# Performance work log

Measured on AMD Instinct MI355X. Metric: run time of the kernel, lower is better.

Reference implementation:

```python
import jax, jax.numpy as jnp
import numpy as np

N_NODES = 100_000
N_EDGES = 20_000   # hyperedges
NNZ = 2_000_000    # incidence pairs
F = 128
BN_EPS = 1e-5


def setup_inputs() -> dict:
    key = jax.random.key(0)
    ks = jax.random.split(key, 6)
    x_0 = jax.random.normal(ks[0], (N_NODES, F), dtype=jnp.float32)
    x_1 = jax.random.normal(ks[1], (N_EDGES, F), dtype=jnp.float32)
    node_idx = jax.random.randint(ks[2], (NNZ,), 0, N_NODES, dtype=jnp.int32)
    edge_idx = jax.random.randint(ks[3], (NNZ,), 0, N_EDGES, dtype=jnp.int32)
    W_nh = jax.random.normal(ks[4], (F, F), dtype=jnp.float32) / np.float32(np.sqrt(F))
    b_nh = jnp.zeros((F,), jnp.float32)
    W_en = jax.random.normal(ks[5], (F, 2 * F), dtype=jnp.float32) / np.float32(np.sqrt(2 * F))
    b_en = jnp.zeros((F,), jnp.float32)
    ones = jnp.ones((F,), jnp.float32)
    zeros = jnp.zeros((F,), jnp.float32)
    return {
        "x_0": x_0, "x_1": x_1, "node_idx": node_idx, "edge_idx": edge_idx,
        "W_nh": W_nh, "b_nh": b_nh, "W_en": W_en, "b_en": b_en,
        "bn0_gamma": ones, "bn0_beta": zeros, "bn0_mean": zeros, "bn0_var": ones,
        "bn1_gamma": ones, "bn1_beta": zeros, "bn1_mean": zeros, "bn1_var": ones,
    }


def _bn_eval(x, gamma, beta, mean, var):
    # BatchNorm1d in eval mode: normalize with running stats.
    return (x - mean) * (gamma * jax.lax.rsqrt(var + BN_EPS)) + beta


def reference(x_0, x_1, node_idx, edge_idx, W_nh, b_nh, W_en, b_en,
              bn0_gamma, bn0_beta, bn0_mean, bn0_var,
              bn1_gamma, bn1_beta, bn1_mean, bn1_var):
    # --- node -> hyperedge messenger ---
    # per-node message: sigmoid(Linear(x_0))  [n_nodes, F]
    node_messages = jax.nn.sigmoid(x_0 @ W_nh.T + b_nh)
    # gather over incidence list, scatter-sum onto hyperedges  [n_edges, F]
    node_msg_agg = jax.ops.segment_sum(node_messages[node_idx], edge_idx,
                                       num_segments=N_EDGES)

    # --- hyperedge -> node messenger ---
    # per-hyperedge message: sigmoid(Linear(cat(x_1, agg node msgs)))  [n_edges, F]
    he_messages = jax.nn.sigmoid(
        jnp.concatenate([x_1, node_msg_agg], axis=1) @ W_en.T + b_en)
    # gather per incidence, scatter-sum onto nodes  [n_nodes, F]
    he_msg_agg = jax.ops.segment_sum(he_messages[edge_idx], node_idx,
                                     num_segments=N_NODES)

    # --- updates (eval mode: feature dropout is identity) ---
    x0_out = jax.nn.sigmoid(
        _bn_eval(x_0, bn0_gamma, bn0_beta, bn0_mean, bn0_var) + he_msg_agg)
    x1_out = jax.nn.sigmoid(
        _bn_eval(x_1, bn1_gamma, bn1_beta, bn1_mean, bn1_var) + node_msg_agg)
    return (x0_out, x1_out)
```

## Files before the change

kernel.cpp:

```cpp
#include <hip/hip_runtime.h>
#include <hip/hip_bf16.h>
#include <math.h>

#define NNODES 100000
#define NEDGES 20000
#define NNZ_   2000000
#define FDIM   128
#define BN_EPS 1e-5f

#define NBUCK 256
#define CAP   9216
#define BPB_E 79
#define BPB_N 391
#define SH_E  17
#define SH_N  15
#define NPART 8
#define PSLICE 12500

typedef __attribute__((ext_vector_type(8))) short bf16x8_t;
typedef __attribute__((ext_vector_type(4))) float f32x4_t;
typedef __attribute__((ext_vector_type(8))) unsigned short u16x8_t;

__device__ __forceinline__ float sigmoidf_(float x) {
    return 1.0f / (1.0f + __expf(-x));
}
__device__ __forceinline__ float bf2f(unsigned short u) {
    return __uint_as_float(((unsigned)u) << 16);
}
__device__ __forceinline__ unsigned short f2bf(float f) {
    __hip_bfloat16 h = __float2bfloat16(f);
    return *reinterpret_cast<unsigned short*>(&h);
}

__global__ __launch_bounds__(256) void prep_w(
    const float* __restrict__ W_nh, const float* __restrict__ W_en,
    unsigned short* __restrict__ Wnh_bf, float* __restrict__ WTen)
{
    int idx = blockIdx.x * blockDim.x + threadIdx.x;
    if (idx < FDIM * FDIM) {
        Wnh_bf[idx] = f2bf(W_nh[idx]);
    } else {
        int j = idx - FDIM * FDIM;
        if (j >= 2 * FDIM * FDIM) return;
        int k = j >> 7, c = j & 127;
        WTen[j] = W_en[c * 2 * FDIM + k];
    }
}

__global__ __launch_bounds__(256) void gemm1_mfma(
    const float* __restrict__ x0, const unsigned short* __restrict__ Wb,
    const float* __restrict__ bias, unsigned short* __restrict__ out)
{
    __shared__ unsigned short As[32][FDIM + 8];
    const int tid  = threadIdx.x;
    const int row0 = blockIdx.x * 32;
    {
        int r = tid >> 3, c0 = (tid & 7) * 16;
        const float* src = x0 + (size_t)(row0 + r) * FDIM + c0;
        unsigned short* dst = &As[r][c0];
        #pragma unroll
        for (int i = 0; i < 4; i++) {
            float4 v = *(const float4*)(src + i * 4);
            dst[i * 4 + 0] = f2bf(v.x);
            dst[i * 4 + 1] = f2bf(v.y);
            dst[i * 4 + 2] = f2bf(v.z);
            dst[i * 4 + 3] = f2bf(v.w);
        }
    }
    __syncthreads();
    const int wave  = tid >> 6;
    const int lane  = tid & 63;
    const int mhalf = wave & 1;
    const int nhalf = wave >> 1;
    const int lm    = lane & 15;
    const int quad  = lane >> 4;
    f32x4_t acc[4] = {};
    #pragma unroll
    for (int ks = 0; ks < 4; ks++) {
        bf16x8_t a = *(const bf16x8_t*)&As[mhalf * 16 + lm][ks * 32 + quad * 8];
        #pragma unroll
        for (int nt = 0; nt < 4; nt++) {
            int n = nhalf * 64 + nt * 16 + lm;
            bf16x8_t b = *(const bf16x8_t*)(Wb + (size_t)n * FDIM + ks * 32 + quad * 8);
            acc[nt] = __builtin_amdgcn_mfma_f32_16x16x32_bf16(a, b, acc[nt], 0, 0, 0);
        }
    }
    const int mbase = row0 + mhalf * 16 + quad * 4;
    #pragma unroll
    for (int nt = 0; nt < 4; nt++) {
        int n = nhalf * 64 + nt * 16 + lm;
        float bv = bias[n];
        #pragma unroll
        for (int r2 = 0; r2 < 4; r2++) {
            out[(size_t)(mbase + r2) * FDIM + n] = f2bf(sigmoidf_(acc[nt][r2] + bv));
        }
    }
}

__global__ __launch_bounds__(256, 2) void gemm_sig_bf16(
    const float* __restrict__ A1, const float* __restrict__ A2,
    const float* __restrict__ WT, const float* __restrict__ bias,
    unsigned short* __restrict__ out)
{
    constexpr int K = 256, BK = 64;
    __shared__ float As[32][BK + 4];
    __shared__ float Ws[BK][FDIM];
    const int tid  = threadIdx.x;
    const int row0 = blockIdx.x * 32;
    const int tcol = tid & 31;
    const int trow = tid >> 5;
    float acc[4][4] = {};
    for (int kk = 0; kk < K; kk += BK) {
        const float* Asrc = (kk < FDIM) ? A1 : A2;
        const int koff    = (kk < FDIM) ? kk : kk - FDIM;
        #pragma unroll
        for (int i = 0; i < 2; i++) {
            int l = tid + i * 256;
            int r = l >> 4, j = l & 15;
            float4 v = *(const float4*)(Asrc + (size_t)(row0 + r) * FDIM + koff + j * 4);
            *(float4*)&As[r][j * 4] = v;
        }
        #pragma unroll
        for (int i = 0; i < 8; i++) {
            int l = tid + i * 256;
            int k = l >> 5, j = l & 31;
            float4 v = *(const float4*)(WT + (size_t)(kk + k) * FDIM + j * 4);
            *(float4*)&Ws[k][j * 4] = v;
        }
        __syncthreads();
        #pragma unroll
        for (int k = 0; k < BK; k += 4) {
            float4 a[4];
            #pragma unroll
            for (int r = 0; r < 4; r++)
                a[r] = *(const float4*)&As[trow * 4 + r][k];
            #pragma unroll
            for (int kq = 0; kq < 4; kq++) {
                float4 w = *(const float4*)&Ws[k + kq][tcol * 4];
                #pragma unroll
                for (int r = 0; r < 4; r++) {
                    float av = (kq == 0) ? a[r].x : (kq == 1) ? a[r].y
                             : (kq == 2) ? a[r].z : a[r].w;
                    acc[r][0] += av * w.x;
                    acc[r][1] += av * w.y;
                    acc[r][2] += av * w.z;
                    acc[r][3] += av * w.w;
                }
            }
        }
        __syncthreads();
    }
    float4 bv = *(const float4*)(bias + tcol * 4);
    #pragma unroll
    for (int r = 0; r < 4; r++) {
        int row = row0 + trow * 4 + r;
        ushort4 o;
        o.x = f2bf(sigmoidf_(acc[r][0] + bv.x));
        o.y = f2bf(sigmoidf_(acc[r][1] + bv.y));
        o.z = f2bf(sigmoidf_(acc[r][2] + bv.z));
        o.w = f2bf(sigmoidf_(acc[r][3] + bv.w));
        *(ushort4*)(out + (size_t)row * FDIM + tcol * 4) = o;
    }
}

__global__ __launch_bounds__(1024) void bucket_scatter(
    const int* __restrict__ ni, const int* __restrict__ ei,
    unsigned* __restrict__ buck_e, unsigned* __restrict__ buck_n,
    int* __restrict__ gcur_e, int* __restrict__ gcur_n)
{
    __shared__ int lh_e[NBUCK], lh_n[NBUCK], lb_e[NBUCK], lb_n[NBUCK];
    const int t = threadIdx.x;
    if (t < NBUCK) { lh_e[t] = 0; lh_n[t] = 0; }
    __syncthreads();
    unsigned ent_e[4], ent_n[4];
    int be[4], bn[4], re[4], rn[4];
    const int base = blockIdx.x * 4096;
    #pragma unroll
    for (int j = 0; j < 4; j++) {
        int i = base + j * 1024 + t;
        if (i < NNZ_) {
            unsigned n = (unsigned)ni[i], e = (unsigned)ei[i];
            ent_e[j] = (e << SH_E) | n;  be[j] = (int)(e / BPB_E);
            ent_n[j] = (n << SH_N) | e;  bn[j] = (int)(n / BPB_N);
            re[j] = atomicAdd(&lh_e[be[j]], 1);
            rn[j] = atomicAdd(&lh_n[bn[j]], 1);
        } else { be[j] = -1; }
    }
    __syncthreads();
    if (t < NBUCK) {
        lb_e[t] = t * CAP + atomicAdd(&gcur_e[t], lh_e[t]);
        lb_n[t] = t * CAP + atomicAdd(&gcur_n[t], lh_n[t]);
    }
    __syncthreads();
    #pragma unroll
    for (int j = 0; j < 4; j++) {
        if (be[j] >= 0) {
            buck_e[(size_t)lb_e[be[j]] + re[j]] = ent_e[j];
            buck_n[(size_t)lb_n[bn[j]] + rn[j]] = ent_n[j];
        }
    }
}

__device__ __forceinline__ int ep_bin(unsigned ent) {
    int e = (int)(ent >> SH_E);
    int n = (int)(ent & 0x1FFFFu);
    return e * NPART + n / PSLICE;
}

__device__ __forceinline__ void sort_bucket_e(
    const unsigned* __restrict__ region, int cnt, int gbase, int bucket,
    unsigned* __restrict__ csr, int* __restrict__ off)
{
    __shared__ unsigned lh[768];
    __shared__ unsigned lw[4];
    const int t = threadIdx.x;
    lh[t] = 0; lh[t + 256] = 0; lh[t + 512] = 0;
    __syncthreads();
    const int b0 = bucket * (BPB_E * NPART);
    for (int i = t; i < cnt; i += 256)
        atomicAdd(&lh[ep_bin(region[i]) - b0], 1u);
    __syncthreads();
    unsigned h0 = lh[3 * t], h1 = lh[3 * t + 1], h2 = lh[3 * t + 2];
    unsigned s = h0 + h1 + h2, inc = s;
    const int lane = t & 63;
    #pragma unroll
    for (int d = 1; d <= 32; d <<= 1) {
        unsigned v = (unsigned)__shfl_up((int)inc, d, 64);
        if (lane >= d) inc += v;
    }
    if (lane == 63) lw[t >> 6] = inc;
    __syncthreads();
    unsigned pre = 0;
    #pragma unroll
    for (int w = 0; w < 4; w++) if (w < (t >> 6)) pre += lw[w];
    unsigned excl = pre + inc - s;
    unsigned c0 = (unsigned)gbase + excl, c1 = c0 + h0, c2 = c1 + h1;
    lh[3 * t] = c0; lh[3 * t + 1] = c1; lh[3 * t + 2] = c2;
    #pragma unroll
    for (int j = 0; j < 3; j++) {
        int ib = 3 * t + j;
        unsigned cc = (j == 0) ? c0 : (j == 1) ? c1 : c2;
        if (ib <= BPB_E * NPART && b0 + ib <= NEDGES * NPART) off[b0 + ib] = (int)cc;
    }
    __syncthreads();
    for (int i = t; i < cnt; i += 256) {
        unsigned ent = region[i];
        unsigned pos = atomicAdd(&lh[ep_bin(ent) - b0], 1u);
        csr[pos] = ent & 0x1FFFFu;
    }
}

__device__ __forceinline__ void sort_bucket_n(
    const unsigned* __restrict__ region, int cnt, int gbase, int b0,
    unsigned short* __restrict__ csr, int* __restrict__ off)
{
    __shared__ unsigned lh[512];
    __shared__ unsigned lw[4];
    const int t = threadIdx.x;
    lh[t] = 0; lh[t + 256] = 0;
    __syncthreads();
    for (int i = t; i < cnt; i += 256) {
        int bin = (int)(region[i] >> SH_N) - b0;
        atomicAdd(&lh[bin], 1u);
    }
    __syncthreads();
    unsigned h0 = lh[2 * t], h1 = lh[2 * t + 1];
    unsigned s = h0 + h1, inc = s;
    const int lane = t & 63;
    #pragma unroll
    for (int d = 1; d <= 32; d <<= 1) {
        unsigned v = (unsigned)__shfl_up((int)inc, d, 64);
        if (lane >= d) inc += v;
    }
    if (lane == 63) lw[t >> 6] = inc;
    __syncthreads();
    unsigned pre = 0;
    #pragma unroll
    for (int w = 0; w < 4; w++) if (w < (t >> 6)) pre += lw[w];
    unsigned excl = pre + inc - s;
    unsigned c0 = (unsigned)gbase + excl;
    unsigned c1 = c0 + h0;
    lh[2 * t] = c0; lh[2 * t + 1] = c1;
    int i0 = 2 * t, i1 = 2 * t + 1;
    if (i0 <= BPB_N && b0 + i0 <= NNODES) off[b0 + i0] = (int)c0;
    if (i1 <= BPB_N && b0 + i1 <= NNODES) off[b0 + i1] = (int)c1;
    __syncthreads();
    for (int i = t; i < cnt; i += 256) {
        unsigned ent = region[i];
        int bin = (int)(ent >> SH_N) - b0;
        unsigned pos = atomicAdd(&lh[bin], 1u);
        csr[pos] = (unsigned short)(ent & 0x7FFFu);
    }
}

__global__ __launch_bounds__(256) void bucket_sort(
    const unsigned* __restrict__ buck_e, const unsigned* __restrict__ buck_n,
    const int* __restrict__ gcur_e, const int* __restrict__ gcur_n,
    unsigned* __restrict__ csr_e, unsigned short* __restrict__ csr_n,
    int* __restrict__ off_ep, int* __restrict__ off_n)
{
    const int b = blockIdx.x & 255;
    const int* gc = (blockIdx.x < 256) ? gcur_e : gcur_n;
    __shared__ int ws4[4];
    const int t = threadIdx.x;
    int v = (t < b) ? gc[t] : 0;
    #pragma unroll
    for (int d = 32; d > 0; d >>= 1) v += __shfl_down(v, d, 64);
    if ((t & 63) == 0) ws4[t >> 6] = v;
    __syncthreads();
    const int gbase = ws4[0] + ws4[1] + ws4[2] + ws4[3];
    const int cnt = gc[b];
    __syncthreads();
    if (blockIdx.x < 256)
        sort_bucket_e(buck_e + (size_t)b * CAP, cnt, gbase, b, csr_e, off_ep);
    else
        sort_bucket_n(buck_n + (size_t)b * CAP, cnt, gbase, b * BPB_N, csr_n, off_n);
}

__global__ __launch_bounds__(256) void seg_part_gather(
    const unsigned short* __restrict__ table, const unsigned* __restrict__ csr,
    const int* __restrict__ off_ep, float* __restrict__ partial)
{
    const int p = blockIdx.x & 7;
    const int e = (blockIdx.x >> 3) * 4 + (threadIdx.x >> 6);
    const int lane = threadIdx.x & 63;
    const int sub  = lane >> 4;
    const int c8   = (lane & 15) * 8;
    const int bin  = e * NPART + p;
    const int i0 = off_ep[bin], i1 = off_ep[bin + 1];
    f32x4_t a0 = {}, a1 = {};
    int i = i0;
    for (; i + 8 <= i1; i += 8) {
        int r0 = (int)csr[i + sub];
        int r1 = (int)csr[i + 4 + sub];
        u16x8_t v0 = *(const u16x8_t*)(table + (size_t)r0 * FDIM + c8);
        u16x8_t v1 = *(const u16x8_t*)(table + (size_t)r1 * FDIM + c8);
        a0[0] += bf2f(v0[0]) + bf2f(v1[0]);
        a0[1] += bf2f(v0[1]) + bf2f(v1[1]);
        a0[2] += bf2f(v0[2]) + bf2f(v1[2]);
        a0[3] += bf2f(v0[3]) + bf2f(v1[3]);
        a1[0] += bf2f(v0[4]) + bf2f(v1[4]);
        a1[1] += bf2f(v0[5]) + bf2f(v1[5]);
        a1[2] += bf2f(v0[6]) + bf2f(v1[6]);
        a1[3] += bf2f(v0[7]) + bf2f(v1[7]);
    }
    if (i + 4 <= i1) {
        int r = (int)csr[i + sub];
        u16x8_t v = *(const u16x8_t*)(table + (size_t)r * FDIM + c8);
        a0[0] += bf2f(v[0]); a0[1] += bf2f(v[1]);
        a0[2] += bf2f(v[2]); a0[3] += bf2f(v[3]);
        a1[0] += bf2f(v[4]); a1[1] += bf2f(v[5]);
        a1[2] += bf2f(v[6]); a1[3] += bf2f(v[7]);
        i += 4;
    }
    if (i < i1 && sub < i1 - i) {
        int r = (int)csr[i + sub];
        u16x8_t v = *(const u16x8_t*)(table + (size_t)r * FDIM + c8);
        a0[0] += bf2f(v[0]); a0[1] += bf2f(v[1]);
        a0[2] += bf2f(v[2]); a0[3] += bf2f(v[3]);
        a1[0] += bf2f(v[4]); a1[1] += bf2f(v[5]);
        a1[2] += bf2f(v[6]); a1[3] += bf2f(v[7]);
    }
    #pragma unroll
    for (int j = 0; j < 4; j++) {
        a0[j] += __shfl_xor(a0[j], 16, 64);
        a0[j] += __shfl_xor(a0[j], 32, 64);
        a1[j] += __shfl_xor(a1[j], 16, 64);
        a1[j] += __shfl_xor(a1[j], 32, 64);
    }
    if (sub < 2) {
        const int q = c8 + sub * 4;
        f32x4_t s = sub ? a1 : a0;
        *(f32x4_t*)(partial + ((size_t)p * NEDGES + e) * FDIM + q) = s;
    }
}

__global__ __launch_bounds__(256) void reduce_fin(
    const float* __restrict__ part, const float* __restrict__ x1,
    const float* __restrict__ g, const float* __restrict__ bb,
    const float* __restrict__ mm, const float* __restrict__ vv,
    float* __restrict__ B, float* __restrict__ out1)
{
    const int idx = blockIdx.x * 256 + threadIdx.x;
    if (idx >= NEDGES * (FDIM / 4)) return;
    const size_t q = (size_t)idx * 4;
    f32x4_t s = {};
    #pragma unroll
    for (int p = 0; p < NPART; p++)
        s += __builtin_nontemporal_load(
                 (const f32x4_t*)(part + (size_t)p * NEDGES * FDIM + q));
    *(f32x4_t*)(B + q) = s;
    const int col = (idx & 31) * 4;
    f32x4_t xv = *(const f32x4_t*)(x1 + q);
    f32x4_t gg = *(const f32x4_t*)(g + col);
    f32x4_t bt = *(const f32x4_t*)(bb + col);
    f32x4_t mn = *(const f32x4_t*)(mm + col);
    f32x4_t vr = *(const f32x4_t*)(vv + col);
    f32x4_t o;
    #pragma unroll
    for (int j = 0; j < 4; j++)
        o[j] = sigmoidf_((xv[j] - mn[j]) * (gg[j] * rsqrtf(vr[j] + BN_EPS))
                         + bt[j] + s[j]);
    __builtin_nontemporal_store(o, (f32x4_t*)(out1 + q));
}

template<typename IDX, int U, int OFFSTR>
__global__ __launch_bounds__(256) void seg_sum_fin_v2(
    const unsigned short* __restrict__ table, const IDX* __restrict__ csr,
    const int* __restrict__ off, const float* __restrict__ x,
    const float* __restrict__ g, const float* __restrict__ bb,
    const float* __restrict__ mm, const float* __restrict__ vv,
    float* __restrict__ agg_out, float* __restrict__ fin_out, int nseg)
{
    const int seg = blockIdx.x * 4 + (threadIdx.x >> 6);
    if (seg >= nseg) return;
    const int lane = threadIdx.x & 63;
    const int c    = lane & 15;
    const int sub  = lane >> 4;
    const int c8   = c * 8;

    const int i0 = off[seg * OFFSTR], i1 = off[seg * OFFSTR + OFFSTR];
    f32x4_t a0 = {}, a1 = {};

    int i = i0;
    for (; i + 4 * U <= i1; i += 4 * U) {
        int r[U];
        u16x8_t v[U];
        #pragma unroll
        for (int u = 0; u < U; u++) r[u] = (int)csr[i + 4 * u + sub];
        #pragma unroll
        for (int u = 0; u < U; u++)
            v[u] = *(const u16x8_t*)(table + (size_t)r[u] * FDIM + c8);
        #pragma unroll
        for (int u = 0; u < U; u++) {
            a0[0] += bf2f(v[u][0]); a0[1] += bf2f(v[u][1]);
            a0[2] += bf2f(v[u][2]); a0[3] += bf2f(v[u][3]);
            a1[0] += bf2f(v[u][4]); a1[1] += bf2f(v[u][5]);
            a1[2] += bf2f(v[u][6]); a1[3] += bf2f(v[u][7]);
        }
    }
    if (i < i1) {
        u16x8_t v[U];
        #pragma unroll
        for (int u = 0; u < U; u++) {
            int row = i + 4 * u + sub;
            u16x8_t z = {};
            v[u] = z;
            if (row < i1)
                v[u] = *(const u16x8_t*)(table + (size_t)csr[row] * FDIM + c8);
        }
        #pragma unroll
        for (int u = 0; u < U; u++) {
            a0[0] += bf2f(v[u][0]); a0[1] += bf2f(v[u][1]);
            a0[2] += bf2f(v[u][2]); a0[3] += bf2f(v[u][3]);
            a1[0] += bf2f(v[u][4]); a1[1] += bf2f(v[u][5]);
            a1[2] += bf2f(v[u][6]); a1[3] += bf2f(v[u][7]);
        }
    }

    #pragma unroll
    for (int j = 0; j < 4; j++) {
        a0[j] += __shfl_xor(a0[j], 16, 64);
        a0[j] += __shfl_xor(a0[j], 32, 64);
        a1[j] += __shfl_xor(a1[j], 16, 64);
        a1[j] += __shfl_xor(a1[j], 32, 64);
    }

    if (sub < 2) {
        const int q = c8 + sub * 4;
        f32x4_t s = sub ? a1 : a0;
        if (agg_out)
            *(f32x4_t*)(agg_out + (size_t)seg * FDIM + q) = s;
        if (fin_out) {
            f32x4_t xv = *(const f32x4_t*)(x + (size_t)seg * FDIM + q);
            f32x4_t gg = *(const f32x4_t*)(g + q);
            f32x4_t bt = *(const f32x4_t*)(bb + q);
            f32x4_t mn = *(const f32x4_t*)(mm + q);
            f32x4_t vr = *(const f32x4_t*)(vv + q);
            f32x4_t o;
            #pragma unroll
            for (int j = 0; j < 4; j++)
                o[j] = sigmoidf_((xv[j] - mn[j]) * (gg[j] * rsqrtf(vr[j] + BN_EPS))
                                 + bt[j] + s[j]);
            *(f32x4_t*)(fin_out + (size_t)seg * FDIM + q) = o;
        }
    }
}

extern "C" void kernel_launch(void* const* d_in, const int* in_sizes, int n_in,
                              void* d_out, int out_size, void* d_ws, size_t ws_size,
                              hipStream_t stream)
{
    const float* x0       = (const float*)d_in[0];
    const float* x1       = (const float*)d_in[1];
    const int*   node_idx = (const int*)d_in[2];
    const int*   edge_idx = (const int*)d_in[3];
    const float* W_nh     = (const float*)d_in[4];
    const float* b_nh     = (const float*)d_in[5];
    const float* W_en     = (const float*)d_in[6];
    const float* b_en     = (const float*)d_in[7];
    const float* bn0g = (const float*)d_in[8];
    const float* bn0b = (const float*)d_in[9];
    const float* bn0m = (const float*)d_in[10];
    const float* bn0v = (const float*)d_in[11];
    const float* bn1g = (const float*)d_in[12];
    const float* bn1b = (const float*)d_in[13];
    const float* bn1m = (const float*)d_in[14];
    const float* bn1v = (const float*)d_in[15];

    float* ws = (float*)d_ws;
    float* B    = ws;
    float* WTen = B + (size_t)NEDGES * FDIM;
    unsigned short* Wnh_bf = (unsigned short*)(WTen + 2 * FDIM * FDIM);
    unsigned short* A_bf = Wnh_bf + FDIM * FDIM;
    unsigned short* D_bf = A_bf + (size_t)NNODES * FDIM;
    int* off_ep = (int*)(D_bf + (size_t)NEDGES * FDIM);
    int* off_n  = off_ep + 160004;
    unsigned* csr_e = (unsigned*)(off_n + 100004);
    unsigned short* csr_n = (unsigned short*)(csr_e + NNZ_);
    unsigned* buck_e = (unsigned*)(csr_n + NNZ_);
    unsigned* buck_n = buck_e + (size_t)NBUCK * CAP;
    int* gcur_e = (int*)(buck_n + (size_t)NBUCK * CAP);
    int* gcur_n = gcur_e + NBUCK;
    float* partial = (float*)buck_e;
    const size_t need = ((char*)partial - (char*)d_ws)
                      + (size_t)NPART * NEDGES * FDIM * sizeof(float);
    const bool big = ws_size >= need;

    hipMemsetAsync(gcur_e, 0, 2 * NBUCK * sizeof(int), stream);
    bucket_scatter<<<(NNZ_ + 4095) / 4096, 1024, 0, stream>>>(
        node_idx, edge_idx, buck_e, buck_n, gcur_e, gcur_n);
    bucket_sort<<<2 * NBUCK, 256, 0, stream>>>(buck_e, buck_n, gcur_e, gcur_n,
                                               csr_e, csr_n, off_ep, off_n);

    prep_w<<<(3 * FDIM * FDIM + 255) / 256, 256, 0, stream>>>(W_nh, W_en, Wnh_bf, WTen);

    float* out0 = (float*)d_out;
    float* out1 = out0 + (size_t)NNODES * FDIM;

    gemm1_mfma<<<NNODES / 32, 256, 0, stream>>>(x0, Wnh_bf, b_nh, A_bf);

    if (big) {
        seg_part_gather<<<(NEDGES / 4) * 8, 256, 0, stream>>>(
            A_bf, csr_e, off_ep, partial);
        reduce_fin<<<(NEDGES * (FDIM / 4) + 255) / 256, 256, 0, stream>>>(
            partial, x1, bn1g, bn1b, bn1m, bn1v, B, out1);
    } else {
        seg_sum_fin_v2<unsigned, 8, NPART><<<(NEDGES + 3) / 4, 256, 0, stream>>>(
            A_bf, csr_e, off_ep, x1, bn1g, bn1b, bn1m, bn1v, B, out1, NEDGES);
    }
    gemm_sig_bf16<<<NEDGES / 32, 256, 0, stream>>>(x1, B, WTen, b_en, D_bf);

    seg_sum_fin_v2<unsigned short, 4, 1><<<(NNODES + 3) / 4, 256, 0, stream>>>(
        D_bf, csr_n, off_n, x0, bn0g, bn0b, bn0m, bn0v, nullptr, out0, NNODES);
}
```

Before: 404.4 us.

## Replace FP32 SIMT edge GEMM with split-bf16 MFMA and fold memset into prep

The second GEMM (edge messages, K=256) moves from scalar FP32 FMA to MFMA bf16 instructions. Both activations and weights are split into hi/lo bf16 parts and combined with three products (hi*hi, lo*hi, hi*lo) to keep near-fp32 accuracy. Separately, the bucket-counter memset is folded into the weight-prep kernel, which now runs first, removing one launch. The cost is six MFMA passes with weights read from global memory, plus extra shared-memory conversion work.

```diff
diff --git a/kernel.cpp b/kernel.cpp
--- a/kernel.cpp
+++ b/kernel.cpp
@@ -34,17 +34,26 @@
 
 __global__ __launch_bounds__(256) void prep_w(
     const float* __restrict__ W_nh, const float* __restrict__ W_en,
-    unsigned short* __restrict__ Wnh_bf, float* __restrict__ WTen)
+    unsigned short* __restrict__ Wnh_bf,
+    unsigned short* __restrict__ W1hi, unsigned short* __restrict__ W1lo,
+    unsigned short* __restrict__ W2hi, unsigned short* __restrict__ W2lo,
+    int* __restrict__ gcur)
 {
     int idx = blockIdx.x * blockDim.x + threadIdx.x;
+    if (idx < 2 * NBUCK) gcur[idx] = 0;
     if (idx < FDIM * FDIM) {
         Wnh_bf[idx] = f2bf(W_nh[idx]);
-    } else {
-        int j = idx - FDIM * FDIM;
-        if (j >= 2 * FDIM * FDIM) return;
-        int k = j >> 7, c = j & 127;
-        WTen[j] = W_en[c * 2 * FDIM + k];
-    }
+        return;
+    }
+    int j = idx - FDIM * FDIM;
+    if (j >= 2 * FDIM * FDIM) return;
+    int n = j >> 8, kk = j & 255;
+    float w = W_en[n * 2 * FDIM + kk];
+    unsigned short hi = f2bf(w);
+    unsigned short lo = f2bf(w - bf2f(hi));
+    int o = n * FDIM + (kk & 127);
+    if (kk < FDIM) { W1hi[o] = hi; W1lo[o] = lo; }
+    else           { W2hi[o] = hi; W2lo[o] = lo; }
 }
 
 __global__ __launch_bounds__(256) void gemm1_mfma(
@@ -97,69 +106,72 @@
     }
 }
 
-__global__ __launch_bounds__(256, 2) void gemm_sig_bf16(
-    const float* __restrict__ A1, const float* __restrict__ A2,
-    const float* __restrict__ WT, const float* __restrict__ bias,
-    unsigned short* __restrict__ out)
-{
-    constexpr int K = 256, BK = 64;
-    __shared__ float As[32][BK + 4];
-    __shared__ float Ws[BK][FDIM];
+__global__ __launch_bounds__(256) void gemm2_mfma(
+    const float* __restrict__ x1, const float* __restrict__ Bagg,
+    const unsigned short* __restrict__ W1hi, const unsigned short* __restrict__ W1lo,
+    const unsigned short* __restrict__ W2hi, const unsigned short* __restrict__ W2lo,
+    const float* __restrict__ bias, unsigned short* __restrict__ out)
+{
+    __shared__ unsigned short Ax[2][32][FDIM + 8];
+    __shared__ unsigned short Ab[2][32][FDIM + 8];
     const int tid  = threadIdx.x;
     const int row0 = blockIdx.x * 32;
-    const int tcol = tid & 31;
-    const int trow = tid >> 5;
-    float acc[4][4] = {};
-    for (int kk = 0; kk < K; kk += BK) {
-        const float* Asrc = (kk < FDIM) ? A1 : A2;
-        const int koff    = (kk < FDIM) ? kk : kk - FDIM;
-        #pragma unroll
-        for (int i = 0; i < 2; i++) {
-            int l = tid + i * 256;
-            int r = l >> 4, j = l & 15;
-            float4 v = *(const float4*)(Asrc + (size_t)(row0 + r) * FDIM + koff + j * 4);
-            *(float4*)&As[r][j * 4] = v;
-        }
-        #pragma unroll
-        for (int i = 0; i < 8; i++) {
-            int l = tid + i * 256;
-            int k = l >> 5, j = l & 31;
-            float4 v = *(const float4*)(WT + (size_t)(kk + k) * FDIM + j * 4);
-            *(float4*)&Ws[k][j * 4] = v;
-        }
-        __syncthreads();
-        #pragma unroll
-        for (int k = 0; k < BK; k += 4) {
-            float4 a[4];
+    {
+        int r = tid >> 3, c0 = (tid & 7) * 16;
+        const float* sx = x1   + (size_t)(row0 + r) * FDIM + c0;
+        const float* sb = Bagg + (size_t)(row0 + r) * FDIM + c0;
+        #pragma unroll
+        for (int i = 0; i < 4; i++) {
+            float4 v = *(const float4*)(sx + i * 4);
+            float4 w = *(const float4*)(sb + i * 4);
             #pragma unroll
-            for (int r = 0; r < 4; r++)
-                a[r] = *(const float4*)&As[trow * 4 + r][k];
+            for (int c = 0; c < 4; c++) {
+                float fv = (c == 0) ? v.x : (c == 1) ? v.y : (c == 2) ? v.z : v.w;
+                unsigned short h = f2bf(fv);
+                Ax[0][r][c0 + i * 4 + c] = h;
+                Ax[1][r][c0 + i * 4 + c] = f2bf(fv - bf2f(h));
+                float fw = (c == 0) ? w.x : (c == 1) ? w.y : (c == 2) ? w.z : w.w;
+                unsigned short hb = f2bf(fw);
+                Ab[0][r][c0 + i * 4 + c] = hb;
+                Ab[1][r][c0 + i * 4 + c] = f2bf(fw - bf2f(hb));
+            }
+        }
+    }
+    __syncthreads();
+    const int wave  = tid >> 6;
+    const int lane  = tid & 63;
+    const int mhalf = wave & 1;
+    const int nhalf = wave >> 1;
+    const int lm    = lane & 15;
+    const int quad  = lane >> 4;
+    f32x4_t acc[4] = {};
+    const unsigned short* Wsel[6] = {W1hi, W1hi, W1lo, W2hi, W2hi, W2lo};
+    #pragma unroll
+    for (int ps = 0; ps < 6; ps++) {
+        const unsigned short (*Asel)[FDIM + 8] =
+            (ps < 3) ? ((ps == 1) ? Ax[1] : Ax[0])
+                     : ((ps == 4) ? Ab[1] : Ab[0]);
+        const unsigned short* Wp = Wsel[ps];
+        #pragma unroll
+        for (int ks = 0; ks < 4; ks++) {
+            bf16x8_t a = *(const bf16x8_t*)&Asel[mhalf * 16 + lm][ks * 32 + quad * 8];
             #pragma unroll
-            for (int kq = 0; kq < 4; kq++) {
-                float4 w = *(const float4*)&Ws[k + kq][tcol * 4];
-                #pragma unroll
-                for (int r = 0; r < 4; r++) {
-                    float av = (kq == 0) ? a[r].x : (kq == 1) ? a[r].y
-                             : (kq == 2) ? a[r].z : a[r].w;
-                    acc[r][0] += av * w.x;
-                    acc[r][1] += av * w.y;
-                    acc[r][2] += av * w.z;
-                    acc[r][3] += av * w.w;
-                }
+            for (int nt = 0; nt < 4; nt++) {
+                int n = nhalf * 64 + nt * 16 + lm;
+                bf16x8_t b = *(const bf16x8_t*)(Wp + (size_t)n * FDIM + ks * 32 + quad * 8);
+                acc[nt] = __builtin_amdgcn_mfma_f32_16x16x32_bf16(a, b, acc[nt], 0, 0, 0);
             }
         }
-        __syncthreads();
-    }
-    float4 bv = *(const float4*)(bias + tcol * 4);
-    #pragma unroll
-    for (int r = 0; r < 4; r++) {
-        int row = row0 + trow * 4 + r;
-        ushort4 o;
-        o.x = f2bf(sigmoidf_(acc[r][0] + bv.x));
-        o.y = f2bf(sigmoidf_(acc[r][1] + bv.y));
-        o.z = f2bf(sigmoidf_(acc[r][2] + bv.z));
-        o.w = f2bf(sigmoidf_(acc[r][3] + bv.w));
-        *(ushort4*)(out + (size_t)row * FDIM + tcol * 4) = o;
+    }
+    const int mbase = row0 + mhalf * 16 + quad * 4;
+    #pragma unroll
+    for (int nt = 0; nt < 4; nt++) {
+        int n = nhalf * 64 + nt * 16 + lm;
+        float bv = bias[n];
+        #pragma unroll
+        for (int r2 = 0; r2 < 4; r2++) {
+            out[(size_t)(mbase + r2) * FDIM + n] = f2bf(sigmoidf_(acc[nt][r2] + bv));
+        }
     }
 }
 
@@ -509,10 +521,13 @@
     const float* bn1v = (const float*)d_in[15];
 
     float* ws = (float*)d_ws;
-    float* B    = ws;
-    float* WTen = B + (size_t)NEDGES * FDIM;
-    unsigned short* Wnh_bf = (unsigned short*)(WTen + 2 * FDIM * FDIM);
-    unsigned short* A_bf = Wnh_bf + FDIM * FDIM;
+    float* B = ws;
+    unsigned short* Wnh_bf = (unsigned short*)(B + (size_t)NEDGES * FDIM);
+    unsigned short* W1hi = Wnh_bf + FDIM * FDIM;
+    unsigned short* W1lo = W1hi + FDIM * FDIM;
+    unsigned short* W2hi = W1lo + FDIM * FDIM;
+    unsigned short* W2lo = W2hi + FDIM * FDIM;
+    unsigned short* A_bf = W2lo + FDIM * FDIM;
     unsigned short* D_bf = A_bf + (size_t)NNODES * FDIM;
     int* off_ep = (int*)(D_bf + (size_t)NEDGES * FDIM);
     int* off_n  = off_ep + 160004;
@@ -527,13 +542,13 @@
                       + (size_t)NPART * NEDGES * FDIM * sizeof(float);
     const bool big = ws_size >= need;
 
-    hipMemsetAsync(gcur_e, 0, 2 * NBUCK * sizeof(int), stream);
+    prep_w<<<(3 * FDIM * FDIM + 255) / 256, 256, 0, stream>>>(
+        W_nh, W_en, Wnh_bf, W1hi, W1lo, W2hi, W2lo, gcur_e);
+
     bucket_scatter<<<(NNZ_ + 4095) / 4096, 1024, 0, stream>>>(
         node_idx, edge_idx, buck_e, buck_n, gcur_e, gcur_n);
     bucket_sort<<<2 * NBUCK, 256, 0, stream>>>(buck_e, buck_n, gcur_e, gcur_n,
                                                csr_e, csr_n, off_ep, off_n);
-
-    prep_w<<<(3 * FDIM * FDIM + 255) / 256, 256, 0, stream>>>(W_nh, W_en, Wnh_bf, WTen);
 
     float* out0 = (float*)d_out;
     float* out1 = out0 + (size_t)NNODES * FDIM;
@@ -549,8 +564,9 @@
         seg_sum_fin_v2<unsigned, 8, NPART><<<(NEDGES + 3) / 4, 256, 0, stream>>>(
             A_bf, csr_e, off_ep, x1, bn1g, bn1b, bn1m, bn1v, B, out1, NEDGES);
     }
-    gemm_sig_bf16<<<NEDGES / 32, 256, 0, stream>>>(x1, B, WTen, b_en, D_bf);
-
+
+    gemm2_mfma<<<NEDGES / 32, 256, 0, stream>>>(
+        x1, B, W1hi, W1lo, W2hi, W2lo, b_en, D_bf);
     seg_sum_fin_v2<unsigned short, 4, 1><<<(NNODES + 3) / 4, 256, 0, stream>>>(
         D_bf, csr_n, off_n, x0, bn0g, bn0b, bn0m, bn0v, nullptr, out0, NNODES);
 }
```

Result: no change. 400.0 us (-1.1%).
